# Kernel optimization log

Hardware: AMD Instinct MI355X
Metric: run time of the kernel (lower is better)

## Reference

```python
import jax, jax.numpy as jnp
import numpy as np

N = 16384
D = 128

def setup_inputs() -> dict:
    key = jax.random.key(0)
    k1, k2 = jax.random.split(key)
    point_cloud1 = jax.random.normal(k1, (1, N, D), dtype=jnp.float32)
    point_cloud2 = jax.random.normal(k2, (1, N, D), dtype=jnp.float32)
    return {"point_cloud1": point_cloud1, "point_cloud2": point_cloud2}

def reference(point_cloud1, point_cloud2):
    # Squared pairwise distances via the expansion ||a-b||^2 = ||a||^2 + ||b||^2 - 2 a.b
    # (mathematically identical to the original broadcast-subtract form, but avoids
    #  materializing the [1, N, N, D] intermediate).
    a2 = jnp.sum(point_cloud1 * point_cloud1, axis=-1)          # [1, N]
    b2 = jnp.sum(point_cloud2 * point_cloud2, axis=-1)          # [1, N]
    ab = jnp.einsum('bnd,bmd->bnm', point_cloud1, point_cloud2) # [1, N, N]
    dists_squared = a2[:, :, None] + b2[:, None, :] - 2.0 * ab  # [1, N, N]
    min_dists1 = jnp.min(dists_squared, axis=2)  # nearest in cloud2 for each point in cloud1
    min_dists2 = jnp.min(dists_squared, axis=1)  # nearest in cloud1 for each point in cloud2
    return jnp.mean(min_dists1) + jnp.mean(min_dists2)
```

## Files before the change

### kernel.cpp

```cpp
#include <hip/hip_runtime.h>
#include <hip/hip_bf16.h>

#define N_PTS 16384
#define DIM   128
#define KAUG  160
#define ROWB  (KAUG * 2)

typedef __bf16 bf16x8 __attribute__((ext_vector_type(8)));
typedef float  f32x4  __attribute__((ext_vector_type(4)));

__device__ __forceinline__ unsigned fmap(float f) {
    unsigned u = __float_as_uint(f);
    return (u & 0x80000000u) ? ~u : (u | 0x80000000u);
}
__device__ __forceinline__ float funmap(unsigned u) {
    return __uint_as_float((u & 0x80000000u) ? (u & 0x7FFFFFFFu) : ~u);
}

__device__ __forceinline__ void gload_lds16(const void* g, void* l) {
    __builtin_amdgcn_global_load_lds(
        (const __attribute__((address_space(1))) void*)g,
        (__attribute__((address_space(3))) void*)l, 16, 0, 0);
}

__global__ void chamfer_prep4(const float* __restrict__ A, const float* __restrict__ B,
                              unsigned short* __restrict__ Ax, unsigned short* __restrict__ Bx,
                              unsigned* __restrict__ minbuf) {
    int gtid = blockIdx.x * 256 + threadIdx.x;
    if (gtid < 4 * N_PTS) minbuf[gtid] = 0xFFFFFFFFu;

    int wave = blockIdx.x * 4 + (threadIdx.x >> 6);
    int lane = threadIdx.x & 63;
    int isB  = wave >= N_PTS;
    int row  = isB ? (wave - N_PTS) : wave;
    const float* src = isB ? B : A;
    unsigned short* dst = isB ? Bx : Ax;

    float2 v = *reinterpret_cast<const float2*>(&src[(size_t)row * DIM + lane * 2]);

    float sc = isB ? 1.f : -2.f;
    __bf16 bx = (__bf16)(sc * v.x), by = (__bf16)(sc * v.y);
    ushort2 st;
    st.x = __builtin_bit_cast(unsigned short, bx);
    st.y = __builtin_bit_cast(unsigned short, by);
    *reinterpret_cast<ushort2*>(&dst[(size_t)row * KAUG + lane * 2]) = st;

    float s = fmaf(v.x, v.x, v.y * v.y);
    #pragma unroll
    for (int off = 1; off < 64; off <<= 1) s += __shfl_xor(s, off);

    __bf16 hb = (__bf16)s;
    float  hf = (float)hb;
    __bf16 lb = (__bf16)(s - hf);
    unsigned short hu = __builtin_bit_cast(unsigned short, hb);
    unsigned short lu = __builtin_bit_cast(unsigned short, lb);
    const unsigned short one = 0x3F80;

    if (lane < 16) {
        ushort2 tw; tw.x = 0; tw.y = 0;
        if (lane == 0) { tw.x = isB ? hu : one; tw.y = isB ? lu : one; }
        if (lane == 1) { tw.x = isB ? one : hu; tw.y = isB ? one : lu; }
        *reinterpret_cast<ushort2*>(&dst[(size_t)row * KAUG + 128 + lane * 2]) = tw;
    }
}

__global__ __launch_bounds__(256, 2)
void chamfer_gemm_min4(const unsigned short* __restrict__ Ax,
                       const unsigned short* __restrict__ Bx,
                       unsigned* __restrict__ rowminS,
                       unsigned* __restrict__ colminS) {
    __shared__ __align__(16) unsigned char sB[2][40960];

    const int b   = blockIdx.x;
    const int tm  = (b >> 2) * 128;
    const int tn0 = (b & 3) * 32;

    const int t = threadIdx.x, w = t >> 6, lane = t & 63;
    const int lq = lane >> 4, lr = lane & 15;
    const int wr = (w >> 1) * 64, wc = (w & 1) * 64;

    bf16x8 af[4][5];
    #pragma unroll
    for (int mi = 0; mi < 4; ++mi)
        #pragma unroll
        for (int ks = 0; ks < 5; ++ks) {
            int row = tm + wr + mi * 16 + lr;
            int kc  = ks * 4 + lq;
            af[mi][ks] = *reinterpret_cast<const bf16x8*>(&Ax[(size_t)row * KAUG + kc * 8]);
        }

    #pragma unroll
    for (int j = 0; j < 10; ++j) {
        int chunk = j * 256 + t;
        int r = chunk / 20;
        int s = chunk - r * 20;
        int c = (s < 16) ? (s ^ (r & 7)) : (16 + ((s - 16) ^ (r & 3)));
        gload_lds16(Bx + (size_t)(tn0 * 128 + r) * KAUG + c * 8, sB[0] + chunk * 16);
    }
    __syncthreads();

    const int own_row = tm + wr + ((lr >> 2) << 4) + (lq << 2) + (lr & 3);
    const int ni_own  = ((lq & 1) << 1) | (lq >> 1);
    float rmin_run = 3.4e38f;

    for (int it = 0; it < 32; ++it) {
        const int cur = it & 1;
        const int tn  = tn0 + it;

        if (it + 1 < 32) {
            #pragma unroll
            for (int j = 0; j < 10; ++j) {
                int chunk = j * 256 + t;
                int r = chunk / 20;
                int s = chunk - r * 20;
                int c = (s < 16) ? (s ^ (r & 7)) : (16 + ((s - 16) ^ (r & 3)));
                gload_lds16(Bx + (size_t)((tn + 1) * 128 + r) * KAUG + c * 8,
                            sB[cur ^ 1] + chunk * 16);
            }
        }

        f32x4 acc[4][4] = {};
        #pragma unroll
        for (int ks = 0; ks < 5; ++ks) {
            bf16x8 bfr[4];
            #pragma unroll
            for (int ni = 0; ni < 4; ++ni) {
                int r = wc + ni * 16 + lr;
                int slot = (ks < 4) ? ((ks * 4 + lq) ^ (r & 7)) : (16 + (lq ^ (r & 3)));
                bfr[ni] = *reinterpret_cast<const bf16x8*>(&sB[cur][r * ROWB + slot * 16]);
            }
            #pragma unroll
            for (int mi = 0; mi < 4; ++mi)
                #pragma unroll
                for (int ni = 0; ni < 4; ++ni)
                    acc[mi][ni] = __builtin_amdgcn_mfma_f32_16x16x32_bf16(af[mi][ks], bfr[ni], acc[mi][ni], 0, 0, 0);
        }

        float v[16];
        #pragma unroll
        for (int mi = 0; mi < 4; ++mi)
            #pragma unroll
            for (int j = 0; j < 4; ++j)
                v[mi * 4 + j] = fminf(fminf(acc[mi][0][j], acc[mi][1][j]),
                                      fminf(acc[mi][2][j], acc[mi][3][j]));
        #pragma unroll
        for (int k = 0; k < 8; ++k) {
            float s = (lr & 8) ? v[k] : v[k + 8];
            float r = __shfl_xor(s, 8);
            v[k] = (lr & 8) ? fminf(v[k + 8], r) : fminf(v[k], r);
        }
        #pragma unroll
        for (int k = 0; k < 4; ++k) {
            float s = (lr & 4) ? v[k] : v[k + 4];
            float r = __shfl_xor(s, 4);
            v[k] = (lr & 4) ? fminf(v[k + 4], r) : fminf(v[k], r);
        }
        #pragma unroll
        for (int k = 0; k < 2; ++k) {
            float s = (lr & 2) ? v[k] : v[k + 2];
            float r = __shfl_xor(s, 2);
            v[k] = (lr & 2) ? fminf(v[k + 2], r) : fminf(v[k], r);
        }
        {
            float s = (lr & 1) ? v[0] : v[1];
            float r = __shfl_xor(s, 1);
            v[0] = (lr & 1) ? fminf(v[1], r) : fminf(v[0], r);
        }
        rmin_run = fminf(rmin_run, v[0]);

        float cp[4];
        #pragma unroll
        for (int ni = 0; ni < 4; ++ni) {
            float m0 = fminf(fminf(acc[0][ni][0], acc[0][ni][1]), fminf(acc[0][ni][2], acc[0][ni][3]));
            float m1 = fminf(fminf(acc[1][ni][0], acc[1][ni][1]), fminf(acc[1][ni][2], acc[1][ni][3]));
            float m2 = fminf(fminf(acc[2][ni][0], acc[2][ni][1]), fminf(acc[2][ni][2], acc[2][ni][3]));
            float m3 = fminf(fminf(acc[3][ni][0], acc[3][ni][1]), fminf(acc[3][ni][2], acc[3][ni][3]));
            cp[ni] = fminf(fminf(m0, m1), fminf(m2, m3));
        }
        #pragma unroll
        for (int k = 0; k < 2; ++k) {
            float s = (lane & 16) ? cp[k] : cp[k + 2];
            float r = __shfl_xor(s, 16);
            cp[k] = (lane & 16) ? fminf(cp[k + 2], r) : fminf(cp[k], r);
        }
        float cfin;
        {
            float s = (lane & 32) ? cp[0] : cp[1];
            float r = __shfl_xor(s, 32);
            cfin = (lane & 32) ? fminf(cp[1], r) : fminf(cp[0], r);
        }
        const int own_col = tn * 128 + wc + ni_own * 16 + lr;

        __syncthreads();

        atomicMin(&colminS[(size_t)(w >> 1) * N_PTS + own_col], fmap(cfin));
    }

    atomicMin(&rowminS[(size_t)(w & 1) * N_PTS + own_row], fmap(rmin_run));
}

__global__ void chamfer_finalize4(const unsigned* __restrict__ rowminS,
                                  const unsigned* __restrict__ colminS,
                                  float* __restrict__ out) {
    __shared__ double sred[16];
    int t = threadIdx.x;
    double s = 0.0;
    for (int i = t; i < N_PTS; i += 1024) {
        unsigned rm = min(rowminS[i], rowminS[i + N_PTS]);
        unsigned cm = min(colminS[i], colminS[i + N_PTS]);
        s += (double)funmap(rm) + (double)funmap(cm);
    }
    #pragma unroll
    for (int off = 32; off; off >>= 1) s += __shfl_down(s, off);
    if ((t & 63) == 0) sred[t >> 6] = s;
    __syncthreads();
    if (t == 0) {
        double tot = 0.0;
        #pragma unroll
        for (int i = 0; i < 16; ++i) tot += sred[i];
        out[0] = (float)(tot * (1.0 / (double)N_PTS));
    }
}

__global__ void chamfer_prep2(const float* __restrict__ A, const float* __restrict__ B,
                              unsigned short* __restrict__ Abf, unsigned short* __restrict__ Bbf,
                              float* __restrict__ a2, float* __restrict__ b2,
                              unsigned* __restrict__ rowmin, unsigned* __restrict__ colmin) {
    int wave = blockIdx.x * 4 + (threadIdx.x >> 6);
    int lane = threadIdx.x & 63;
    int isB  = wave >= N_PTS;
    int row  = isB ? (wave - N_PTS) : wave;
    const float* src = isB ? B : A;
    unsigned short* dst = isB ? Bbf : Abf;

    float2 v = *reinterpret_cast<const float2*>(&src[(size_t)row * DIM + lane * 2]);
    __bf16 bx = (__bf16)v.x, by = (__bf16)v.y;
    ushort2 st;
    st.x = __builtin_bit_cast(unsigned short, bx);
    st.y = __builtin_bit_cast(unsigned short, by);
    *reinterpret_cast<ushort2*>(&dst[(size_t)row * DIM + lane * 2]) = st;

    float s = fmaf(v.x, v.x, v.y * v.y);
    #pragma unroll
    for (int off = 32; off; off >>= 1) s += __shfl_down(s, off);
    if (lane == 0) {
        if (isB) { b2[row] = s; colmin[row] = 0xFFFFFFFFu; }
        else     { a2[row] = s; rowmin[row] = 0xFFFFFFFFu; }
    }
}

__global__ __launch_bounds__(512, 2)
void chamfer_gemm_min3(const unsigned short* __restrict__ Abf, const unsigned short* __restrict__ Bbf,
                       const float* __restrict__ a2, const float* __restrict__ b2,
                       unsigned* __restrict__ rowmin, unsigned* __restrict__ colmin) {
    __shared__ __align__(16) unsigned char sA[65536];
    __shared__ __align__(16) unsigned char sB2[2][32768];

    const int b = blockIdx.x;
    const int tm_base = (b >> 2) * 256;
    const int tn0 = (b & 3) * 32;

    const int t = threadIdx.x;
    const int w = t >> 6, lane = t & 63;
    const int lq = lane >> 4, lr = lane & 15;
    const int wr = (w >> 1) * 64;
    const int wc = (w & 1) * 64;

    #pragma unroll
    for (int j = 0; j < 8; ++j) {
        int chunk = ((w << 3) + j) * 64 + lane;
        int r = chunk >> 4, kc = (chunk & 15) ^ (r & 7);
        gload_lds16(Abf + (size_t)(tm_base + r) * DIM + kc * 8, sA + chunk * 16);
    }
    #pragma unroll
    for (int j = 0; j < 4; ++j) {
        int chunk = ((w << 2) + j) * 64 + lane;
        int r = chunk >> 4, kc = (chunk & 15) ^ (r & 7);
        gload_lds16(Bbf + (size_t)(tn0 * 128 + r) * DIM + kc * 8, sB2[0] + chunk * 16);
    }

    float a2v[4][4];
    #pragma unroll
    for (int mi = 0; mi < 4; ++mi) {
        float4 q = *reinterpret_cast<const float4*>(&a2[tm_base + wr + mi * 16 + lq * 4]);
        a2v[mi][0] = q.x; a2v[mi][1] = q.y; a2v[mi][2] = q.z; a2v[mi][3] = q.w;
    }
    __syncthreads();

    for (int it = 0; it < 32; ++it) {
        const int cur = it & 1;
        const int tn = tn0 + it;

        if (it + 1 < 32) {
            #pragma unroll
            for (int j = 0; j < 4; ++j) {
                int chunk = ((w << 2) + j) * 64 + lane;
                int r = chunk >> 4, kc = (chunk & 15) ^ (r & 7);
                gload_lds16(Bbf + (size_t)((tn + 1) * 128 + r) * DIM + kc * 8,
                            sB2[cur ^ 1] + chunk * 16);
            }
        }

        f32x4 acc[4][4] = {};
        #pragma unroll
        for (int ks = 0; ks < 4; ++ks) {
            const int kc = ks * 4 + lq;
            bf16x8 af2[4], bfr[4];
            #pragma unroll
            for (int mi = 0; mi < 4; ++mi) {
                int r = wr + mi * 16 + lr;
                af2[mi] = *reinterpret_cast<const bf16x8*>(&sA[r * 256 + ((kc * 16) ^ ((r & 7) << 4))]);
            }
            #pragma unroll
            for (int ni = 0; ni < 4; ++ni) {
                int r = wc + ni * 16 + lr;
                bfr[ni] = *reinterpret_cast<const bf16x8*>(&sB2[cur][r * 256 + ((kc * 16) ^ ((r & 7) << 4))]);
            }
            #pragma unroll
            for (int mi = 0; mi < 4; ++mi)
                #pragma unroll
                for (int ni = 0; ni < 4; ++ni)
                    acc[mi][ni] = __builtin_amdgcn_mfma_f32_16x16x32_bf16(af2[mi], bfr[ni], acc[mi][ni], 0, 0, 0);
        }

        const int col_base = tn * 128 + wc;
        float b2v[4];
        #pragma unroll
        for (int ni = 0; ni < 4; ++ni) b2v[ni] = b2[col_base + ni * 16 + lr];

        float v[16];
        #pragma unroll
        for (int mi = 0; mi < 4; ++mi) {
            #pragma unroll
            for (int j = 0; j < 4; ++j) {
                float m = fmaf(-2.f, acc[mi][0][j], b2v[0]);
                m = fminf(m, fmaf(-2.f, acc[mi][1][j], b2v[1]));
                m = fminf(m, fmaf(-2.f, acc[mi][2][j], b2v[2]));
                m = fminf(m, fmaf(-2.f, acc[mi][3][j], b2v[3]));
                v[mi * 4 + j] = m;
            }
        }
        #pragma unroll
        for (int k = 0; k < 8; ++k) {
            float s = (lr & 8) ? v[k] : v[k + 8];
            float r = __shfl_xor(s, 8);
            v[k] = (lr & 8) ? fminf(v[k + 8], r) : fminf(v[k], r);
        }
        #pragma unroll
        for (int k = 0; k < 4; ++k) {
            float s = (lr & 4) ? v[k] : v[k + 4];
            float r = __shfl_xor(s, 4);
            v[k] = (lr & 4) ? fminf(v[k + 4], r) : fminf(v[k], r);
        }
        #pragma unroll
        for (int k = 0; k < 2; ++k) {
            float s = (lr & 2) ? v[k] : v[k + 2];
            float r = __shfl_xor(s, 2);
            v[k] = (lr & 2) ? fminf(v[k + 2], r) : fminf(v[k], r);
        }
        {
            float s = (lr & 1) ? v[0] : v[1];
            float r = __shfl_xor(s, 1);
            v[0] = (lr & 1) ? fminf(v[1], r) : fminf(v[0], r);
        }
        const int own_row = tm_base + wr + ((lr >> 2) << 4) + (lq << 2) + (lr & 3);

        float cp[4];
        #pragma unroll
        for (int ni = 0; ni < 4; ++ni) {
            float m = fmaf(-2.f, acc[0][ni][0], a2v[0][0]);
            #pragma unroll
            for (int mi = 0; mi < 4; ++mi)
                #pragma unroll
                for (int j = 0; j < 4; ++j)
                    if (mi | j) m = fminf(m, fmaf(-2.f, acc[mi][ni][j], a2v[mi][j]));
            cp[ni] = m;
        }
        #pragma unroll
        for (int k = 0; k < 2; ++k) {
            float s = (lane & 16) ? cp[k] : cp[k + 2];
            float r = __shfl_xor(s, 16);
            cp[k] = (lane & 16) ? fminf(cp[k + 2], r) : fminf(cp[k], r);
        }
        float cfin;
        {
            float s = (lane & 32) ? cp[0] : cp[1];
            float r = __shfl_xor(s, 32);
            cfin = (lane & 32) ? fminf(cp[1], r) : fminf(cp[0], r);
        }
        const int ni_own = ((lq & 1) << 1) | (lq >> 1);
        const int own_col = col_base + ni_own * 16 + lr;

        __syncthreads();

        atomicMin(&rowmin[own_row], fmap(v[0]));
        atomicMin(&colmin[own_col], fmap(cfin));
    }
}

__global__ void chamfer_finalize2(const unsigned* __restrict__ rowmin,
                                  const unsigned* __restrict__ colmin,
                                  const float* __restrict__ a2, const float* __restrict__ b2,
                                  float* __restrict__ out) {
    __shared__ double sred[16];
    int t = threadIdx.x;
    double s = 0.0;
    for (int i = t; i < N_PTS; i += 1024)
        s += ((double)funmap(rowmin[i]) + (double)a2[i])
           + ((double)funmap(colmin[i]) + (double)b2[i]);
    #pragma unroll
    for (int off = 32; off; off >>= 1) s += __shfl_down(s, off);
    if ((t & 63) == 0) sred[t >> 6] = s;
    __syncthreads();
    if (t == 0) {
        double tot = 0.0;
        #pragma unroll
        for (int i = 0; i < 16; ++i) tot += sred[i];
        out[0] = (float)(tot * (1.0 / (double)N_PTS));
    }
}

extern "C" void kernel_launch(void* const* d_in, const int* in_sizes, int n_in,
                              void* d_out, int out_size, void* d_ws, size_t ws_size,
                              hipStream_t stream) {
    const float* A = (const float*)d_in[0];
    const float* B = (const float*)d_in[1];
    float* out = (float*)d_out;
    char* ws = (char*)d_ws;

    const size_t SZ4   = (size_t)N_PTS * KAUG * sizeof(unsigned short);
    const size_t need4 = 2 * SZ4 + 4 * (size_t)N_PTS * 4;

    const size_t BF    = (size_t)N_PTS * DIM * sizeof(unsigned short);
    const size_t need3 = 2 * BF + 4 * (size_t)(1 << 16);

    if (ws_size >= need4) {
        unsigned short* Ax = (unsigned short*)(ws);
        unsigned short* Bx = (unsigned short*)(ws + SZ4);
        unsigned* minbuf   = (unsigned*)(ws + 2 * SZ4);
        unsigned* rowminS  = minbuf;
        unsigned* colminS  = minbuf + 2 * N_PTS;

        chamfer_prep4<<<(2 * N_PTS) / 4, 256, 0, stream>>>(A, B, Ax, Bx, minbuf);
        chamfer_gemm_min4<<<512, 256, 0, stream>>>(Ax, Bx, rowminS, colminS);
        chamfer_finalize4<<<1, 1024, 0, stream>>>(rowminS, colminS, out);
    } else if (ws_size >= need3) {
        unsigned short* Abf = (unsigned short*)(ws);
        unsigned short* Bbf = (unsigned short*)(ws + BF);
        float*    a2     = (float*)(ws + 2 * BF);
        float*    b2     = (float*)(ws + 2 * BF + (1 << 16));
        unsigned* rowmin = (unsigned*)(ws + 2 * BF + (2 << 16));
        unsigned* colmin = (unsigned*)(ws + 2 * BF + (3 << 16));

        chamfer_prep2<<<(2 * N_PTS) / 4, 256, 0, stream>>>(A, B, Abf, Bbf, a2, b2, rowmin, colmin);
        chamfer_gemm_min3<<<256, 512, 0, stream>>>(Abf, Bbf, a2, b2, rowmin, colmin);
        chamfer_finalize2<<<1, 1024, 0, stream>>>(rowmin, colmin, a2, b2, out);
    }
}
```

Measured before the change: 106.1 us.

## Switch to 32x32x16 MFMA, shrink augmented K to 144, defer row-min reduction

Replaces the 16x16x32 bf16 MFMA tiling with 32x32x16 MFMA tiles, with each wave computing 2x2 tiles of 32x32. It also shrinks the augmented K dimension from 160 to 144, which cuts padding, MFMA work and LDS/global traffic by about a tenth. Row minima are now kept per register across all iterations and reduced with shuffles once at the end, instead of a full shuffle tree on every iteration. The cost is higher register pressure from 32 running-min registers plus the larger accumulators, which may affect occupancy at 2 blocks per CU.

Result: faster. 102.1 us (-3.8%).

```diff
diff --git a/kernel.cpp b/kernel.cpp
--- a/kernel.cpp
+++ b/kernel.cpp
@@ -3,11 +3,13 @@
 
 #define N_PTS 16384
 #define DIM   128
-#define KAUG  160
+#define KAUG  144
 #define ROWB  (KAUG * 2)
+#define NCHUNK 18
 
 typedef __bf16 bf16x8 __attribute__((ext_vector_type(8)));
 typedef float  f32x4  __attribute__((ext_vector_type(4)));
+typedef float  f32x16 __attribute__((ext_vector_type(16)));
 
 __device__ __forceinline__ unsigned fmap(float f) {
     unsigned u = __float_as_uint(f);
@@ -23,7 +25,7 @@
         (__attribute__((address_space(3))) void*)l, 16, 0, 0);
 }
 
-__global__ void chamfer_prep4(const float* __restrict__ A, const float* __restrict__ B,
+__global__ void chamfer_prep5(const float* __restrict__ A, const float* __restrict__ B,
                               unsigned short* __restrict__ Ax, unsigned short* __restrict__ Bx,
                               unsigned* __restrict__ minbuf) {
     int gtid = blockIdx.x * 256 + threadIdx.x;
@@ -56,7 +58,7 @@
     unsigned short lu = __builtin_bit_cast(unsigned short, lb);
     const unsigned short one = 0x3F80;
 
-    if (lane < 16) {
+    if (lane < 8) {
         ushort2 tw; tw.x = 0; tw.y = 0;
         if (lane == 0) { tw.x = isB ? hu : one; tw.y = isB ? lu : one; }
         if (lane == 1) { tw.x = isB ? one : hu; tw.y = isB ? one : lu; }
@@ -65,138 +67,120 @@
 }
 
 __global__ __launch_bounds__(256, 2)
-void chamfer_gemm_min4(const unsigned short* __restrict__ Ax,
+void chamfer_gemm_min5(const unsigned short* __restrict__ Ax,
                        const unsigned short* __restrict__ Bx,
                        unsigned* __restrict__ rowminS,
                        unsigned* __restrict__ colminS) {
-    __shared__ __align__(16) unsigned char sB[2][40960];
+    __shared__ __align__(16) unsigned char sB[2][36864];
 
     const int b   = blockIdx.x;
     const int tm  = (b >> 2) * 128;
     const int tn0 = (b & 3) * 32;
 
     const int t = threadIdx.x, w = t >> 6, lane = t & 63;
-    const int lq = lane >> 4, lr = lane & 15;
+    const int ll = lane & 31, hi = lane >> 5;
     const int wr = (w >> 1) * 64, wc = (w & 1) * 64;
 
-    bf16x8 af[4][5];
-    #pragma unroll
-    for (int mi = 0; mi < 4; ++mi)
-        #pragma unroll
-        for (int ks = 0; ks < 5; ++ks) {
-            int row = tm + wr + mi * 16 + lr;
-            int kc  = ks * 4 + lq;
-            af[mi][ks] = *reinterpret_cast<const bf16x8*>(&Ax[(size_t)row * KAUG + kc * 8]);
-        }
-
-    #pragma unroll
-    for (int j = 0; j < 10; ++j) {
+    bf16x8 af[2][9];
+    #pragma unroll
+    for (int mi = 0; mi < 2; ++mi) {
+        const unsigned short* ap = Ax + (size_t)(tm + wr + mi * 32 + ll) * KAUG + hi * 8;
+        #pragma unroll
+        for (int ks = 0; ks < 9; ++ks)
+            af[mi][ks] = *reinterpret_cast<const bf16x8*>(ap + ks * 16);
+    }
+
+    int goff[9];
+    #pragma unroll
+    for (int j = 0; j < 9; ++j) {
         int chunk = j * 256 + t;
-        int r = chunk / 20;
-        int s = chunk - r * 20;
-        int c = (s < 16) ? (s ^ (r & 7)) : (16 + ((s - 16) ^ (r & 3)));
-        gload_lds16(Bx + (size_t)(tn0 * 128 + r) * KAUG + c * 8, sB[0] + chunk * 16);
+        int r = chunk / NCHUNK;
+        int s = chunk - r * NCHUNK;
+        int c = (s < 16) ? (s ^ (r & 7)) : (16 + ((s - 16) ^ (r & 1)));
+        goff[j] = r * KAUG + c * 8;
+    }
+
+    {
+        const unsigned short* bp = Bx + (size_t)tn0 * 128 * KAUG;
+        #pragma unroll
+        for (int j = 0; j < 9; ++j)
+            gload_lds16(bp + goff[j], sB[0] + (j * 256 + t) * 16);
     }
     __syncthreads();
 
-    const int own_row = tm + wr + ((lr >> 2) << 4) + (lq << 2) + (lr & 3);
-    const int ni_own  = ((lq & 1) << 1) | (lq >> 1);
-    float rmin_run = 3.4e38f;
+    float rmin_part[32];
+    #pragma unroll
+    for (int k = 0; k < 32; ++k) rmin_part[k] = 3.4e38f;
+
+    const int rA = wc + ll;
+    const int rB = wc + 32 + ll;
 
     for (int it = 0; it < 32; ++it) {
         const int cur = it & 1;
         const int tn  = tn0 + it;
 
         if (it + 1 < 32) {
-            #pragma unroll
-            for (int j = 0; j < 10; ++j) {
-                int chunk = j * 256 + t;
-                int r = chunk / 20;
-                int s = chunk - r * 20;
-                int c = (s < 16) ? (s ^ (r & 7)) : (16 + ((s - 16) ^ (r & 3)));
-                gload_lds16(Bx + (size_t)((tn + 1) * 128 + r) * KAUG + c * 8,
-                            sB[cur ^ 1] + chunk * 16);
-            }
-        }
-
-        f32x4 acc[4][4] = {};
-        #pragma unroll
-        for (int ks = 0; ks < 5; ++ks) {
-            bf16x8 bfr[4];
-            #pragma unroll
-            for (int ni = 0; ni < 4; ++ni) {
-                int r = wc + ni * 16 + lr;
-                int slot = (ks < 4) ? ((ks * 4 + lq) ^ (r & 7)) : (16 + (lq ^ (r & 3)));
-                bfr[ni] = *reinterpret_cast<const bf16x8*>(&sB[cur][r * ROWB + slot * 16]);
-            }
-            #pragma unroll
-            for (int mi = 0; mi < 4; ++mi)
-                #pragma unroll
-                for (int ni = 0; ni < 4; ++ni)
-                    acc[mi][ni] = __builtin_amdgcn_mfma_f32_16x16x32_bf16(af[mi][ks], bfr[ni], acc[mi][ni], 0, 0, 0);
-        }
-
-        float v[16];
-        #pragma unroll
-        for (int mi = 0; mi < 4; ++mi)
-            #pragma unroll
-            for (int j = 0; j < 4; ++j)
-                v[mi * 4 + j] = fminf(fminf(acc[mi][0][j], acc[mi][1][j]),
-                                      fminf(acc[mi][2][j], acc[mi][3][j]));
-        #pragma unroll
-        for (int k = 0; k < 8; ++k) {
-            float s = (lr & 8) ? v[k] : v[k + 8];
-            float r = __shfl_xor(s, 8);
-            v[k] = (lr & 8) ? fminf(v[k + 8], r) : fminf(v[k], r);
-        }
-        #pragma unroll
-        for (int k = 0; k < 4; ++k) {
-            float s = (lr & 4) ? v[k] : v[k + 4];
-            float r = __shfl_xor(s, 4);
-            v[k] = (lr & 4) ? fminf(v[k + 4], r) : fminf(v[k], r);
-        }
-        #pragma unroll
-        for (int k = 0; k < 2; ++k) {
-            float s = (lr & 2) ? v[k] : v[k + 2];
-            float r = __shfl_xor(s, 2);
-            v[k] = (lr & 2) ? fminf(v[k + 2], r) : fminf(v[k], r);
-        }
-        {
-            float s = (lr & 1) ? v[0] : v[1];
-            float r = __shfl_xor(s, 1);
-            v[0] = (lr & 1) ? fminf(v[1], r) : fminf(v[0], r);
-        }
-        rmin_run = fminf(rmin_run, v[0]);
-
-        float cp[4];
-        #pragma unroll
-        for (int ni = 0; ni < 4; ++ni) {
-            float m0 = fminf(fminf(acc[0][ni][0], acc[0][ni][1]), fminf(acc[0][ni][2], acc[0][ni][3]));
-            float m1 = fminf(fminf(acc[1][ni][0], acc[1][ni][1]), fminf(acc[1][ni][2], acc[1][ni][3]));
-            float m2 = fminf(fminf(acc[2][ni][0], acc[2][ni][1]), fminf(acc[2][ni][2], acc[2][ni][3]));
-            float m3 = fminf(fminf(acc[3][ni][0], acc[3][ni][1]), fminf(acc[3][ni][2], acc[3][ni][3]));
-            cp[ni] = fminf(fminf(m0, m1), fminf(m2, m3));
-        }
-        #pragma unroll
-        for (int k = 0; k < 2; ++k) {
-            float s = (lane & 16) ? cp[k] : cp[k + 2];
-            float r = __shfl_xor(s, 16);
-            cp[k] = (lane & 16) ? fminf(cp[k + 2], r) : fminf(cp[k], r);
-        }
-        float cfin;
-        {
-            float s = (lane & 32) ? cp[0] : cp[1];
-            float r = __shfl_xor(s, 32);
-            cfin = (lane & 32) ? fminf(cp[1], r) : fminf(cp[0], r);
-        }
-        const int own_col = tn * 128 + wc + ni_own * 16 + lr;
+            const unsigned short* bp = Bx + (size_t)(tn + 1) * 128 * KAUG;
+            #pragma unroll
+            for (int j = 0; j < 9; ++j)
+                gload_lds16(bp + goff[j], sB[cur ^ 1] + (j * 256 + t) * 16);
+        }
+
+        f32x16 acc[2][2] = {};
+        #pragma unroll
+        for (int ks = 0; ks < 9; ++ks) {
+            const int c = ks * 2 + hi;
+            const int sA0 = (c < 16) ? (c ^ (rA & 7)) : (16 + ((c - 16) ^ (rA & 1)));
+            const int sB1 = (c < 16) ? (c ^ (rB & 7)) : (16 + ((c - 16) ^ (rB & 1)));
+            bf16x8 b0 = *reinterpret_cast<const bf16x8*>(&sB[cur][rA * ROWB + sA0 * 16]);
+            bf16x8 b1 = *reinterpret_cast<const bf16x8*>(&sB[cur][rB * ROWB + sB1 * 16]);
+            #pragma unroll
+            for (int mi = 0; mi < 2; ++mi) {
+                acc[mi][0] = __builtin_amdgcn_mfma_f32_32x32x16_bf16(af[mi][ks], b0, acc[mi][0], 0, 0, 0);
+                acc[mi][1] = __builtin_amdgcn_mfma_f32_32x32x16_bf16(af[mi][ks], b1, acc[mi][1], 0, 0, 0);
+            }
+        }
+
+        #pragma unroll
+        for (int mi = 0; mi < 2; ++mi)
+            #pragma unroll
+            for (int reg = 0; reg < 16; ++reg)
+                rmin_part[mi * 16 + reg] =
+                    fminf(rmin_part[mi * 16 + reg], fminf(acc[mi][0][reg], acc[mi][1][reg]));
+
+        float cm0 = acc[0][0][0], cm1 = acc[0][1][0];
+        #pragma unroll
+        for (int mi = 0; mi < 2; ++mi)
+            #pragma unroll
+            for (int reg = 0; reg < 16; ++reg) {
+                if (mi | reg) {
+                    cm0 = fminf(cm0, acc[mi][0][reg]);
+                    cm1 = fminf(cm1, acc[mi][1][reg]);
+                }
+            }
+        cm0 = fminf(cm0, __shfl_xor(cm0, 32));
+        cm1 = fminf(cm1, __shfl_xor(cm1, 32));
+        float cmSel = hi ? cm1 : cm0;
+        const int own_col = tn * 128 + wc + hi * 32 + ll;
 
         __syncthreads();
 
-        atomicMin(&colminS[(size_t)(w >> 1) * N_PTS + own_col], fmap(cfin));
-    }
-
-    atomicMin(&rowminS[(size_t)(w & 1) * N_PTS + own_row], fmap(rmin_run));
+        atomicMin(&colminS[(size_t)(w >> 1) * N_PTS + own_col], fmap(cmSel));
+    }
+
+    #pragma unroll
+    for (int s = 16; s >= 1; s >>= 1) {
+        #pragma unroll
+        for (int k = 0; k < 16; ++k) {
+            if (k < s) {
+                float snd = (ll & s) ? rmin_part[k] : rmin_part[k + s];
+                float r = __shfl_xor(snd, s);
+                rmin_part[k] = (ll & s) ? fminf(rmin_part[k + s], r) : fminf(rmin_part[k], r);
+            }
+        }
+    }
+    const int own_row = tm + wr + ((ll >> 4) << 5) + (ll & 3) + (((ll >> 2) & 3) << 3) + (hi << 2);
+    atomicMin(&rowminS[(size_t)(w & 1) * N_PTS + own_row], fmap(rmin_part[0]));
 }
 
 __global__ void chamfer_finalize4(const unsigned* __restrict__ rowminS,
@@ -428,21 +412,21 @@
     float* out = (float*)d_out;
     char* ws = (char*)d_ws;
 
-    const size_t SZ4   = (size_t)N_PTS * KAUG * sizeof(unsigned short);
-    const size_t need4 = 2 * SZ4 + 4 * (size_t)N_PTS * 4;
+    const size_t SZ5   = (size_t)N_PTS * KAUG * sizeof(unsigned short);
+    const size_t need5 = 2 * SZ5 + 4 * (size_t)N_PTS * 4;
 
     const size_t BF    = (size_t)N_PTS * DIM * sizeof(unsigned short);
     const size_t need3 = 2 * BF + 4 * (size_t)(1 << 16);
 
-    if (ws_size >= need4) {
+    if (ws_size >= need5) {
         unsigned short* Ax = (unsigned short*)(ws);
-        unsigned short* Bx = (unsigned short*)(ws + SZ4);
-        unsigned* minbuf   = (unsigned*)(ws + 2 * SZ4);
+        unsigned short* Bx = (unsigned short*)(ws + SZ5);
+        unsigned* minbuf   = (unsigned*)(ws + 2 * SZ5);
         unsigned* rowminS  = minbuf;
         unsigned* colminS  = minbuf + 2 * N_PTS;
 
-        chamfer_prep4<<<(2 * N_PTS) / 4, 256, 0, stream>>>(A, B, Ax, Bx, minbuf);
-        chamfer_gemm_min4<<<512, 256, 0, stream>>>(Ax, Bx, rowminS, colminS);
+        chamfer_prep5<<<(2 * N_PTS) / 4, 256, 0, stream>>>(A, B, Ax, Bx, minbuf);
+        chamfer_gemm_min5<<<512, 256, 0, stream>>>(Ax, Bx, rowminS, colminS);
         chamfer_finalize4<<<1, 1024, 0, stream>>>(rowminS, colminS, out);
     } else if (ws_size >= need3) {
         unsigned short* Abf = (unsigned short*)(ws);
```
